# Kernel tuning notes

Measured on AMD Instinct MI355X. Metric: run time of the kernel, lower is better.

## Reference

```python
import jax, jax.numpy as jnp
import numpy as np

WINDOW = 33  # must match init_kwargs window_size (odd)


def setup_inputs() -> dict:
    key = jax.random.key(0)
    kq, kk, kv, km = jax.random.split(key, 4)
    B, S, D = 4, 2048, 256
    query = jax.random.normal(kq, (B, S, D), dtype=jnp.float32)
    k = jax.random.normal(kk, (B, S, D), dtype=jnp.float32)
    value = jax.random.normal(kv, (B, S, D), dtype=jnp.float32)
    mask = jax.random.randint(km, (B, S), 0, 2).astype(jnp.int32)
    return {"query": query, "key": k, "value": value, "mask": mask}


def reference(query, key, value, mask):
    # Local (sliding-window) attention, window centered at each position.
    B, S, D = query.shape
    half = WINDOW // 2
    offs = jnp.arange(-half, half + 1)                 # [W]
    idx = jnp.arange(S)[:, None] + offs[None, :]       # [S, W]
    valid = (idx >= 0) & (idx < S)                     # in-bounds window entries
    idxc = jnp.clip(idx, 0, S - 1)
    k_win = key[:, idxc]                               # [B, S, W, D]
    v_win = value[:, idxc]                             # [B, S, W, D]
    scores = jnp.einsum('bsd,bswd->bsw', query, k_win) / jnp.sqrt(jnp.float32(D))
    m_win = (mask[:, idxc] != 0) & valid[None]         # [B, S, W]
    scores = jnp.where(m_win, scores, jnp.float32(-1e10))  # masked_fill(-1e10)
    p_attn = jax.nn.softmax(scores, axis=-1)           # [B, S, W]
    values = jnp.einsum('bsw,bswd->bsd', p_attn, v_win)
    return values, p_attn
```

## Files before the change

### kernel.cpp

```cpp
#include <hip/hip_runtime.h>

#define S_LEN 2048
#define D_DIM 256
#define WIN 33
#define HALF 16
#define VR_STRIDE 266
#define SC_STRIDE 68
#define PT_STRIDE 72

typedef __attribute__((ext_vector_type(8))) short short8_t;
typedef __attribute__((ext_vector_type(4))) float f32x4;

__device__ inline unsigned short f32_to_bf16(float f) {
    unsigned u = __float_as_uint(f);
    return (unsigned short)((u + 0x7fffu + ((u >> 16) & 1u)) >> 16);
}
__device__ inline unsigned pack2_bf16(float lo, float hi) {
    unsigned a = __float_as_uint(lo) + 0x8000u;
    unsigned b = __float_as_uint(hi) + 0x8000u;
    return __builtin_amdgcn_perm(b, a, 0x07060302);
}
__device__ inline short8_t pack_bf16x8(float4 x, float4 y) {
    union { unsigned u[4]; short8_t s; } r;
    r.u[0] = pack2_bf16(x.x, x.y); r.u[1] = pack2_bf16(x.z, x.w);
    r.u[2] = pack2_bf16(y.x, y.y); r.u[3] = pack2_bf16(y.z, y.w);
    return r.s;
}

__global__ __launch_bounds__(256) void local_attn_v5(
    const float* __restrict__ q,
    const float* __restrict__ k,
    const float* __restrict__ v,
    const int*   __restrict__ mask,
    float* __restrict__ out_v,
    float* __restrict__ out_p)
{
    __shared__ __align__(16) unsigned short Vr[48 * VR_STRIDE];
    __shared__ __align__(16) float          Sc[16 * SC_STRIDE];
    __shared__ __align__(16) unsigned short Pt[16 * PT_STRIDE];
    __shared__ int wm[64];

    const int t    = threadIdx.x;
    const int lane = t & 63;
    const int w    = t >> 6;
    const int l15  = lane & 15;
    const int q4   = lane >> 4;

    const int bid  = blockIdx.x;
    const int tile = ((bid & 7) << 6) | (bid >> 3);
    const int b    = tile >> 7;
    const int s0   = (tile & 127) << 4;

    const float* qb = q + ((size_t)b * S_LEN + s0) * D_DIM;
    const float* kb = k + (size_t)b * S_LEN * D_DIM;
    const float* vb = v + (size_t)b * S_LEN * D_DIM;

    float4 vreg[12];
#pragma unroll
    for (int it = 0; it < 12; ++it) {
        const int lin = it * 256 + t;
        const int g   = lin >> 6;
        const int c4  = lin & 63;
        const int idx = min(max(s0 - HALF + g, 0), S_LEN - 1);
        vreg[it] = *(const float4*)(vb + (size_t)idx * D_DIM + c4 * 4);
    }
    if (t < 64) {
        const int idx = s0 - HALF + t;
        wm[t] = (idx >= 0 && idx < S_LEN) ? (mask[b * S_LEN + idx] != 0) : 0;
    }

    if (w < 3) {
        const int c    = 16 * w + l15;
        const int kidx = min(max(s0 - HALF + c, 0), S_LEN - 1);
        const float* kr = kb + (size_t)kidx * D_DIM;
        const float* qr = qb + l15 * D_DIM;
        f32x4 acc = (f32x4){0.f, 0.f, 0.f, 0.f};
#pragma unroll
        for (int ks = 0; ks < 8; ++ks) {
            const float* pq = qr + ks * 32 + q4 * 8;
            const float* pk = kr + ks * 32 + q4 * 8;
            const short8_t aq = pack_bf16x8(*(const float4*)pq, *(const float4*)(pq + 4));
            const short8_t bk = pack_bf16x8(*(const float4*)pk, *(const float4*)(pk + 4));
            acc = __builtin_amdgcn_mfma_f32_16x16x32_bf16(aq, bk, acc, 0, 0, 0);
        }
#pragma unroll
        for (int r = 0; r < 4; ++r)
            Sc[(q4 * 4 + r) * SC_STRIDE + c] = acc[r];
    }

#pragma unroll
    for (int it = 0; it < 12; ++it) {
        const int lin = it * 256 + t;
        const int g   = lin >> 6;
        const int c4  = lin & 63;
        const unsigned u0 = pack2_bf16(vreg[it].x, vreg[it].y);
        const unsigned u1 = pack2_bf16(vreg[it].z, vreg[it].w);
        *(unsigned*)&Vr[g * VR_STRIDE + c4 * 4]     = u0;
        *(unsigned*)&Vr[g * VR_STRIDE + c4 * 4 + 2] = u1;
    }
    __syncthreads();

    {
        const int row = t >> 4;
        const int e   = t & 15;
        float vs[4], ps[4];
        if (e < 12) {
            const float4 s4 = *(const float4*)&Sc[row * SC_STRIDE + 4 * e];
            const float sarr[4] = {s4.x, s4.y, s4.z, s4.w};
#pragma unroll
            for (int kq = 0; kq < 4; ++kq) {
                const int c = 4 * e + kq, j = c - row;
                const bool inb = (j >= 0) && (j < WIN);
                vs[kq] = inb ? (wm[c] ? sarr[kq] * 0.0625f : -1e10f) : -1e30f;
            }
        } else {
#pragma unroll
            for (int kq = 0; kq < 4; ++kq) vs[kq] = -1e30f;
        }
        float m = fmaxf(fmaxf(vs[0], vs[1]), fmaxf(vs[2], vs[3]));
        m = fmaxf(m, __shfl_xor(m, 1, 64));
        m = fmaxf(m, __shfl_xor(m, 2, 64));
        m = fmaxf(m, __shfl_xor(m, 4, 64));
        m = fmaxf(m, __shfl_xor(m, 8, 64));
        float s = 0.f;
#pragma unroll
        for (int kq = 0; kq < 4; ++kq) { vs[kq] = __expf(vs[kq] - m); s += vs[kq]; }
        s += __shfl_xor(s, 1, 64);
        s += __shfl_xor(s, 2, 64);
        s += __shfl_xor(s, 4, 64);
        s += __shfl_xor(s, 8, 64);
        const float rinv = 1.0f / s;
        union { unsigned short u[4]; uint2 d; } pw;
#pragma unroll
        for (int kq = 0; kq < 4; ++kq) {
            ps[kq]   = vs[kq] * rinv;
            pw.u[kq] = f32_to_bf16(ps[kq]);
        }
        *(uint2*)&Pt[row * PT_STRIDE + 4 * e] = pw.d;
        float* prow = out_p + ((size_t)(b * S_LEN + s0 + row)) * WIN;
#pragma unroll
        for (int kq = 0; kq < 4; ++kq) {
            const int j = 4 * e + kq - row;
            if (j >= 0 && j < WIN) prow[j] = ps[kq];
        }
    }
    __syncthreads();

    const short8_t ap0 = *(const short8_t*)&Pt[l15 * PT_STRIDE + q4 * 8];
    const short8_t ap1 = *(const short8_t*)&Pt[l15 * PT_STRIDE + 32 + q4 * 8];
    float* ob = out_v + ((size_t)b * S_LEN + s0) * D_DIM;
#pragma unroll
    for (int nt = 0; nt < 4; ++nt) {
        const int d = 64 * w + 16 * nt + l15;
        short8_t b0, b1;
#pragma unroll
        for (int j = 0; j < 8; ++j)
            b0[j] = (short)Vr[(q4 * 8 + j) * VR_STRIDE + d];
#pragma unroll
        for (int j = 0; j < 8; ++j) {
            const int g = min(32 + q4 * 8 + j, 47);
            b1[j] = (short)Vr[g * VR_STRIDE + d];
        }
        f32x4 acc = (f32x4){0.f, 0.f, 0.f, 0.f};
        acc = __builtin_amdgcn_mfma_f32_16x16x32_bf16(ap0, b0, acc, 0, 0, 0);
        acc = __builtin_amdgcn_mfma_f32_16x16x32_bf16(ap1, b1, acc, 0, 0, 0);
#pragma unroll
        for (int r = 0; r < 4; ++r)
            ob[(size_t)(q4 * 4 + r) * D_DIM + d] = acc[r];
    }
}

extern "C" void kernel_launch(void* const* d_in, const int* in_sizes, int n_in,
                              void* d_out, int out_size, void* d_ws, size_t ws_size,
                              hipStream_t stream) {
    const float* q    = (const float*)d_in[0];
    const float* k    = (const float*)d_in[1];
    const float* v    = (const float*)d_in[2];
    const int*   mask = (const int*)d_in[3];

    const int B = 4;
    float* out_v = (float*)d_out;
    float* out_p = (float*)d_out + (size_t)B * S_LEN * D_DIM;

    const int blocks = B * (S_LEN / 16);
    local_attn_v5<<<blocks, 256, 0, stream>>>(q, k, v, mask, out_v, out_p);
}
```

Measured before the change: 87.02 us.

## Process 32 query rows per 512-thread block and load V directly into MFMA registers

Each block now covers 32 query rows with 8 waves instead of 16 rows with 4 waves. The K window of 64 rows is shared by two row tiles, which cuts the redundant K/V halo traffic per output row. The LDS staging of V in bf16 is removed: each lane gathers its MFMA B-operand values straight from global memory with strided scalar loads and packs them in registers. This saves LDS space and one shared-memory round trip, but the V loads become uncoalesced 4-byte column gathers and register pressure per thread rises.

```diff
diff --git a/kernel.cpp b/kernel.cpp
--- a/kernel.cpp
+++ b/kernel.cpp
@@ -4,7 +4,8 @@
 #define D_DIM 256
 #define WIN 33
 #define HALF 16
-#define VR_STRIDE 266
+#define TROWS 32
+#define SPAN 64
 #define SC_STRIDE 68
 #define PT_STRIDE 72
 
@@ -27,7 +28,7 @@
     return r.s;
 }
 
-__global__ __launch_bounds__(256) void local_attn_v5(
+__global__ __launch_bounds__(512) void local_attn_v6(
     const float* __restrict__ q,
     const float* __restrict__ k,
     const float* __restrict__ v,
@@ -35,45 +36,37 @@
     float* __restrict__ out_v,
     float* __restrict__ out_p)
 {
-    __shared__ __align__(16) unsigned short Vr[48 * VR_STRIDE];
-    __shared__ __align__(16) float          Sc[16 * SC_STRIDE];
-    __shared__ __align__(16) unsigned short Pt[16 * PT_STRIDE];
-    __shared__ int wm[64];
+    __shared__ __align__(16) float          Sc[TROWS * SC_STRIDE];
+    __shared__ __align__(16) unsigned short Pt[TROWS * PT_STRIDE];
+    __shared__ int wm[SPAN];
 
     const int t    = threadIdx.x;
     const int lane = t & 63;
     const int w    = t >> 6;
     const int l15  = lane & 15;
     const int q4   = lane >> 4;
+    const int rt   = w >> 2;
+    const int wq   = w & 3;
 
     const int bid  = blockIdx.x;
-    const int tile = ((bid & 7) << 6) | (bid >> 3);
-    const int b    = tile >> 7;
-    const int s0   = (tile & 127) << 4;
+    const int tile = ((bid & 7) << 5) | (bid >> 3);
+    const int b    = tile >> 6;
+    const int s0   = (tile & 63) << 5;
 
     const float* qb = q + ((size_t)b * S_LEN + s0) * D_DIM;
     const float* kb = k + (size_t)b * S_LEN * D_DIM;
     const float* vb = v + (size_t)b * S_LEN * D_DIM;
 
-    float4 vreg[12];
-#pragma unroll
-    for (int it = 0; it < 12; ++it) {
-        const int lin = it * 256 + t;
-        const int g   = lin >> 6;
-        const int c4  = lin & 63;
-        const int idx = min(max(s0 - HALF + g, 0), S_LEN - 1);
-        vreg[it] = *(const float4*)(vb + (size_t)idx * D_DIM + c4 * 4);
-    }
-    if (t < 64) {
+    if (t < SPAN) {
         const int idx = s0 - HALF + t;
         wm[t] = (idx >= 0 && idx < S_LEN) ? (mask[b * S_LEN + idx] != 0) : 0;
     }
 
-    if (w < 3) {
-        const int c    = 16 * w + l15;
+    {
+        const int c    = wq * 16 + l15;
         const int kidx = min(max(s0 - HALF + c, 0), S_LEN - 1);
         const float* kr = kb + (size_t)kidx * D_DIM;
-        const float* qr = qb + l15 * D_DIM;
+        const float* qr = qb + (size_t)(rt * 16 + l15) * D_DIM;
         f32x4 acc = (f32x4){0.f, 0.f, 0.f, 0.f};
 #pragma unroll
         for (int ks = 0; ks < 8; ++ks) {
@@ -85,37 +78,50 @@
         }
 #pragma unroll
         for (int r = 0; r < 4; ++r)
-            Sc[(q4 * 4 + r) * SC_STRIDE + c] = acc[r];
+            Sc[(rt * 16 + q4 * 4 + r) * SC_STRIDE + c] = acc[r];
     }
 
+    short8_t bv[4][2];
+    {
+        float vr[4][2][8];
 #pragma unroll
-    for (int it = 0; it < 12; ++it) {
-        const int lin = it * 256 + t;
-        const int g   = lin >> 6;
-        const int c4  = lin & 63;
-        const unsigned u0 = pack2_bf16(vreg[it].x, vreg[it].y);
-        const unsigned u1 = pack2_bf16(vreg[it].z, vreg[it].w);
-        *(unsigned*)&Vr[g * VR_STRIDE + c4 * 4]     = u0;
-        *(unsigned*)&Vr[g * VR_STRIDE + c4 * 4 + 2] = u1;
+        for (int dct = 0; dct < 4; ++dct) {
+            const int d = wq * 64 + dct * 16 + l15;
+#pragma unroll
+            for (int ks = 0; ks < 2; ++ks)
+#pragma unroll
+                for (int j = 0; j < 8; ++j) {
+                    const int g   = ks * 32 + q4 * 8 + j;
+                    const int idx = min(max(s0 - HALF + g, 0), S_LEN - 1);
+                    vr[dct][ks][j] = vb[(size_t)idx * D_DIM + d];
+                }
+        }
+#pragma unroll
+        for (int dct = 0; dct < 4; ++dct)
+#pragma unroll
+            for (int ks = 0; ks < 2; ++ks) {
+                float4 x, y;
+                x.x = vr[dct][ks][0]; x.y = vr[dct][ks][1];
+                x.z = vr[dct][ks][2]; x.w = vr[dct][ks][3];
+                y.x = vr[dct][ks][4]; y.y = vr[dct][ks][5];
+                y.z = vr[dct][ks][6]; y.w = vr[dct][ks][7];
+                bv[dct][ks] = pack_bf16x8(x, y);
+            }
     }
     __syncthreads();
 
     {
         const int row = t >> 4;
         const int e   = t & 15;
-        float vs[4], ps[4];
-        if (e < 12) {
-            const float4 s4 = *(const float4*)&Sc[row * SC_STRIDE + 4 * e];
-            const float sarr[4] = {s4.x, s4.y, s4.z, s4.w};
+        const float4 s4 = *(const float4*)&Sc[row * SC_STRIDE + 4 * e];
+        const float sarr[4] = {s4.x, s4.y, s4.z, s4.w};
+        float vs[4];
 #pragma unroll
-            for (int kq = 0; kq < 4; ++kq) {
-                const int c = 4 * e + kq, j = c - row;
-                const bool inb = (j >= 0) && (j < WIN);
-                vs[kq] = inb ? (wm[c] ? sarr[kq] * 0.0625f : -1e10f) : -1e30f;
-            }
-        } else {
-#pragma unroll
-            for (int kq = 0; kq < 4; ++kq) vs[kq] = -1e30f;
+        for (int kq = 0; kq < 4; ++kq) {
+            const int c = 4 * e + kq;
+            const int j = c - row;
+            const bool inb = (j >= 0) && (j < WIN);
+            vs[kq] = inb ? (wm[c] ? sarr[kq] * 0.0625f : -1e10f) : -1e30f;
         }
         float m = fmaxf(fmaxf(vs[0], vs[1]), fmaxf(vs[2], vs[3]));
         m = fmaxf(m, __shfl_xor(m, 1, 64));
@@ -130,13 +136,15 @@
         s += __shfl_xor(s, 4, 64);
         s += __shfl_xor(s, 8, 64);
         const float rinv = 1.0f / s;
-        union { unsigned short u[4]; uint2 d; } pw;
+
+        float ps[4];
+        union { unsigned short u[4]; uint2 d2; } pw;
 #pragma unroll
         for (int kq = 0; kq < 4; ++kq) {
             ps[kq]   = vs[kq] * rinv;
             pw.u[kq] = f32_to_bf16(ps[kq]);
         }
-        *(uint2*)&Pt[row * PT_STRIDE + 4 * e] = pw.d;
+        *(uint2*)&Pt[row * PT_STRIDE + 4 * e] = pw.d2;
         float* prow = out_p + ((size_t)(b * S_LEN + s0 + row)) * WIN;
 #pragma unroll
         for (int kq = 0; kq < 4; ++kq) {
@@ -146,27 +154,20 @@
     }
     __syncthreads();
 
-    const short8_t ap0 = *(const short8_t*)&Pt[l15 * PT_STRIDE + q4 * 8];
-    const short8_t ap1 = *(const short8_t*)&Pt[l15 * PT_STRIDE + 32 + q4 * 8];
-    float* ob = out_v + ((size_t)b * S_LEN + s0) * D_DIM;
+    {
+        const short8_t ap0 = *(const short8_t*)&Pt[(rt * 16 + l15) * PT_STRIDE + q4 * 8];
+        const short8_t ap1 = *(const short8_t*)&Pt[(rt * 16 + l15) * PT_STRIDE + 32 + q4 * 8];
+        float* ob = out_v + ((size_t)b * S_LEN + s0) * D_DIM;
 #pragma unroll
-    for (int nt = 0; nt < 4; ++nt) {
-        const int d = 64 * w + 16 * nt + l15;
-        short8_t b0, b1;
+        for (int dct = 0; dct < 4; ++dct) {
+            f32x4 acc = (f32x4){0.f, 0.f, 0.f, 0.f};
+            acc = __builtin_amdgcn_mfma_f32_16x16x32_bf16(ap0, bv[dct][0], acc, 0, 0, 0);
+            acc = __builtin_amdgcn_mfma_f32_16x16x32_bf16(ap1, bv[dct][1], acc, 0, 0, 0);
+            const int d = wq * 64 + dct * 16 + l15;
 #pragma unroll
-        for (int j = 0; j < 8; ++j)
-            b0[j] = (short)Vr[(q4 * 8 + j) * VR_STRIDE + d];
-#pragma unroll
-        for (int j = 0; j < 8; ++j) {
-            const int g = min(32 + q4 * 8 + j, 47);
-            b1[j] = (short)Vr[g * VR_STRIDE + d];
+            for (int r = 0; r < 4; ++r)
+                ob[(size_t)(rt * 16 + q4 * 4 + r) * D_DIM + d] = acc[r];
         }
-        f32x4 acc = (f32x4){0.f, 0.f, 0.f, 0.f};
-        acc = __builtin_amdgcn_mfma_f32_16x16x32_bf16(ap0, b0, acc, 0, 0, 0);
-        acc = __builtin_amdgcn_mfma_f32_16x16x32_bf16(ap1, b1, acc, 0, 0, 0);
-#pragma unroll
-        for (int r = 0; r < 4; ++r)
-            ob[(size_t)(q4 * 4 + r) * D_DIM + d] = acc[r];
     }
 }
 
@@ -182,6 +183,6 @@
     float* out_v = (float*)d_out;
     float* out_p = (float*)d_out + (size_t)B * S_LEN * D_DIM;
 
-    const int blocks = B * (S_LEN / 16);
-    local_attn_v5<<<blocks, 256, 0, stream>>>(q, k, v, mask, out_v, out_p);
+    const int blocks = B * (S_LEN / TROWS);
+    local_attn_v6<<<blocks, 512, 0, stream>>>(q, k, v, mask, out_v, out_p);
 }
```

After: 83.53 us. 1.04x faster.
